# Kernel tuning notes

Measured on AMD Instinct MI355X. Metric: run time of the kernel, lower is better.

Reference implementation:

```python
import jax, jax.numpy as jnp
import numpy as np

T, B, D = 512, 16, 2048


def setup_inputs() -> dict:
    key = jax.random.key(0)
    k1, k2, k3, k4, k5 = jax.random.split(key, 5)
    scale = 1.0 / np.sqrt(D)  # keep tanh pre-activations in a sane range
    return {
        "h0": jax.random.normal(k1, (B, D), dtype=jnp.float32),
        "x": jax.random.normal(k2, (T, B, D), dtype=jnp.float32),
        "Wx": jax.random.normal(k3, (D, D), dtype=jnp.float32) * scale,
        "Wh": jax.random.normal(k4, (D, D), dtype=jnp.float32) * scale,
        "Wo": jax.random.normal(k5, (D, D), dtype=jnp.float32) * scale,
    }


def reference(h0, x, Wx, Wh, Wo):
    # ONNX Scan with 1 state var, 1 scan input (axis 0, forward direction),
    # 1 scan output (stacked on axis 0, forward direction), 3 outer vars.
    # Body: h' = tanh(x_t @ Wx + h @ Wh); y_t = h' @ Wo
    def step(h, x_t):
        h_new = jnp.tanh(x_t @ Wx + h @ Wh)   # [B, D]
        y_t = h_new @ Wo                      # [B, D]
        return h_new, y_t

    h_final, ys = jax.lax.scan(step, h0, x)   # ys: [T, B, D]
    return (h_final, ys)
```

## Files before the change

### kernel.cpp

```cpp
#include <hip/hip_runtime.h>
#include <hip/hip_bf16.h>

#define DD 2048
#define TT 512
#define NBLK 64
#define HF_SLOT 32768
#define KT 64
#define FSTRIDE 16

typedef __attribute__((ext_vector_type(4))) float  f32x4;
typedef __attribute__((ext_vector_type(8))) short  bf16x8;
typedef __attribute__((ext_vector_type(8))) unsigned short u16x8;
typedef unsigned short ushort_t;
typedef unsigned long long u64_t;

__device__ __forceinline__ void gld_lds16(const void* g, void* l) {
    __builtin_amdgcn_global_load_lds(
        (const __attribute__((address_space(1))) unsigned int*)g,
        (__attribute__((address_space(3))) unsigned int*)l, 16, 0, 0);
}

__device__ __forceinline__ ushort_t f2bf(float v) {
    __hip_bfloat16 h = __float2bfloat16(v);
    return *(ushort_t*)&h;
}

__device__ __forceinline__ u64_t llc_load64(const u64_t* p) {
    return __hip_atomic_load(p, __ATOMIC_RELAXED, __HIP_MEMORY_SCOPE_AGENT);
}
__device__ __forceinline__ void llc_store64(u64_t* p, u64_t v) {
    __hip_atomic_store(p, v, __ATOMIC_RELAXED, __HIP_MEMORY_SCOPE_AGENT);
}
__device__ __forceinline__ unsigned llc_load32(const unsigned* p) {
    return __hip_atomic_load(p, __ATOMIC_RELAXED, __HIP_MEMORY_SCOPE_AGENT);
}
__device__ __forceinline__ float llc_loadf(const float* p) {
    return __hip_atomic_load(p, __ATOMIC_RELAXED, __HIP_MEMORY_SCOPE_AGENT);
}

__global__ void conv_frag(const float* __restrict__ src, ushort_t* __restrict__ dst) {
    int id = blockIdx.x * 256 + threadIdx.x;
    int l  = id & 63;
    int sk = (id >> 6) & 63;
    int mt = id >> 12;
    const float* s = src + (size_t)(mt * 16 + (l & 15)) * DD + sk * 32 + ((l >> 4) * 8);
    float4 a = *(const float4*)s;
    float4 b = *(const float4*)(s + 4);
    u16x8 r;
    r[0] = f2bf(a.x); r[1] = f2bf(a.y); r[2] = f2bf(a.z); r[3] = f2bf(a.w);
    r[4] = f2bf(b.x); r[5] = f2bf(b.y); r[6] = f2bf(b.z); r[7] = f2bf(b.w);
    *(u16x8*)(dst + (size_t)id * 8) = r;
}

__global__ void conv_wt(const float* __restrict__ W, ushort_t* __restrict__ Wt) {
    int id = blockIdx.x * 256 + threadIdx.x;
    int n  = id & (DD - 1);
    int k8 = id >> 11;
    u16x8 r;
#pragma unroll
    for (int j = 0; j < 8; ++j)
        r[j] = f2bf(W[(size_t)(k8 * 8 + j) * DD + n]);
    *(u16x8*)(Wt + (size_t)n * DD + k8 * 8) = r;
}

__global__ __launch_bounds__(256) void gemm_frag(
    const ushort_t* __restrict__ Af, const ushort_t* __restrict__ Bt,
    float* __restrict__ C) {
    __shared__ ushort_t lA[8 * 64 * 8];
    __shared__ ushort_t lB[8 * 64 * 8];
    int tid = threadIdx.x;
    int w = tid >> 6, l = tid & 63;
    int wm = w >> 1, wn = w & 1;
    int quad = l >> 4, col = l & 15;
    int mt0 = blockIdx.x * 8;
    int n0  = blockIdx.y * 128;

    f32x4 acc[4][4] = {};

    for (int sk = 0; sk < KT; ++sk) {
        __syncthreads();
#pragma unroll
        for (int q = 0; q < 2; ++q) {
            int i = w * 2 + q;
            const ushort_t* ga = Af + ((size_t)((mt0 + i) * 64 + sk) * 64 + l) * 8;
            gld_lds16(ga, &lA[i * 512]);
            int jt = i;
            const ushort_t* gb = Bt + (size_t)(n0 + jt * 16 + col) * DD + sk * 32 + quad * 8;
            gld_lds16(gb, &lB[jt * 512]);
        }
        __syncthreads();
        bf16x8 af[4], bf[4];
#pragma unroll
        for (int i = 0; i < 4; ++i) af[i] = *(const bf16x8*)&lA[((wm * 4 + i) * 64 + l) * 8];
#pragma unroll
        for (int j = 0; j < 4; ++j) bf[j] = *(const bf16x8*)&lB[((wn * 4 + j) * 64 + l) * 8];
#pragma unroll
        for (int i = 0; i < 4; ++i)
#pragma unroll
            for (int j = 0; j < 4; ++j)
                acc[i][j] = __builtin_amdgcn_mfma_f32_16x16x32_bf16(af[i], bf[j], acc[i][j], 0, 0, 0);
    }

#pragma unroll
    for (int i = 0; i < 4; ++i)
#pragma unroll
        for (int j = 0; j < 4; ++j) {
            int rg0 = (mt0 + wm * 4 + i) * 16 + quad * 4;
            int cg  = n0 + (wn * 4 + j) * 16 + col;
#pragma unroll
            for (int r = 0; r < 4; ++r)
                C[(size_t)(rg0 + r) * DD + cg] = acc[i][j][r];
        }
}

__global__ __launch_bounds__(256, 1) void rnn_fused(
    const ushort_t* __restrict__ Wht,
    const ushort_t* __restrict__ Wot,
    ushort_t* __restrict__ Hf,
    const float* __restrict__ A32,
    float* __restrict__ out,
    unsigned* __restrict__ flags) {
    __shared__ ushort_t lW[4 * 16 * 2 * 512];
    __shared__ float scr[2048];
    __shared__ ushort_t hstage[512];
    int tid = threadIdx.x;
    int w = tid >> 6, l = tid & 63;
    int quad = l >> 4, col = l & 15;
    bool is_rnn = blockIdx.x < NBLK;
    int b = is_rnn ? blockIdx.x : blockIdx.x - NBLK;
    int c0 = b * 32;
    float* ys = out + HF_SLOT;

    const ushort_t* Wsrc = is_rnn ? Wht : Wot;
#pragma unroll
    for (int s = 0; s < 16; ++s) {
        int sk = w * 16 + s;
#pragma unroll
        for (int jt = 0; jt < 2; ++jt) {
            const ushort_t* gb = Wsrc + (size_t)(c0 + jt * 16 + col) * DD + sk * 32 + quad * 8;
            gld_lds16(gb, &lW[((w * 16 + s) * 2 + jt) << 9]);
        }
    }
    __syncthreads();

    for (int t = 1; t <= TT; ++t) {
        float av[4];
        if (is_rnn && w < 2) {
#pragma unroll
            for (int r = 0; r < 4; ++r)
                av[r] = llc_loadf(&A32[(size_t)((t - 1) * 16 + quad * 4 + r) * DD + c0 + w * 16 + col]);
        }

        unsigned tgt = is_rnn ? (unsigned)(t - 1) : (unsigned)t;
        if (w == 3) {
            unsigned f;
            do {
                f = llc_load32(&flags[l * FSTRIDE]);
            } while (!__all((int)(f >= tgt)));
        }
        __syncthreads();

        const ushort_t* hsrc = Hf + (size_t)(is_rnn ? t - 1 : t) * HF_SLOT;
        bf16x8 hv[16];
#pragma unroll
        for (int s = 0; s < 16; ++s) {
            int sk = w * 16 + s;
            const u64_t* p = (const u64_t*)(hsrc + (size_t)(sk * 64 + l) * 8);
            union { u64_t q[2]; bf16x8 v; } u;
            u.q[0] = llc_load64(p);
            u.q[1] = llc_load64(p + 1);
            hv[s] = u.v;
        }

        f32x4 acc0 = {0.f, 0.f, 0.f, 0.f};
        f32x4 acc1 = {0.f, 0.f, 0.f, 0.f};
#pragma unroll
        for (int s = 0; s < 16; ++s) {
            bf16x8 w0 = *(const bf16x8*)&lW[(((w * 16 + s) * 2 + 0) << 9) + l * 8];
            bf16x8 w1 = *(const bf16x8*)&lW[(((w * 16 + s) * 2 + 1) << 9) + l * 8];
            acc0 = __builtin_amdgcn_mfma_f32_16x16x32_bf16(hv[s], w0, acc0, 0, 0, 0);
            acc1 = __builtin_amdgcn_mfma_f32_16x16x32_bf16(hv[s], w1, acc1, 0, 0, 0);
        }
        *(f32x4*)&scr[((w * 2 + 0) * 64 + l) * 4] = acc0;
        *(f32x4*)&scr[((w * 2 + 1) * 64 + l) * 4] = acc1;
        __syncthreads();

        if (w < 2) {
            int jt = w;
            f32x4 p0 = *(f32x4*)&scr[((0 * 2 + jt) * 64 + l) * 4];
            f32x4 p1 = *(f32x4*)&scr[((1 * 2 + jt) * 64 + l) * 4];
            f32x4 p2 = *(f32x4*)&scr[((2 * 2 + jt) * 64 + l) * 4];
            f32x4 p3 = *(f32x4*)&scr[((3 * 2 + jt) * 64 + l) * 4];
            int lc = jt * 16 + col;
            if (is_rnn) {
                int q2 = lc >> 3, jj = lc & 7;
#pragma unroll
                for (int r = 0; r < 4; ++r) {
                    int m = quad * 4 + r;
                    float x = p0[r] + p1[r] + p2[r] + p3[r] + av[r];
                    float e2 = __expf(-2.f * fabsf(x));
                    float th = copysignf((1.f - e2) / (1.f + e2), x);
                    hstage[(q2 * 16 + m) * 8 + jj] = f2bf(th);
                    if (t == TT) out[(size_t)m * DD + c0 + lc] = th;
                }
            } else {
#pragma unroll
                for (int r = 0; r < 4; ++r) {
                    int m = quad * 4 + r;
                    float y = p0[r] + p1[r] + p2[r] + p3[r];
                    ys[(size_t)((t - 1) * 16 + m) * DD + c0 + lc] = y;
                }
            }
        }

        if (is_rnn) {
            __syncthreads();
            if (w == 0) {
                u64_t* dst = (u64_t*)(Hf + (size_t)t * HF_SLOT + (size_t)(c0 >> 5) * 512);
                const u64_t* s = (const u64_t*)hstage;
                llc_store64(dst + l,      s[l]);
                llc_store64(dst + 64 + l, s[64 + l]);
                __builtin_amdgcn_s_waitcnt(0);
                if (l == 0)
                    __hip_atomic_store(&flags[b * FSTRIDE], (unsigned)t,
                                       __ATOMIC_RELAXED, __HIP_MEMORY_SCOPE_AGENT);
            }
        }
    }
}

extern "C" void kernel_launch(void* const* d_in, const int* in_sizes, int n_in,
                              void* d_out, int out_size, void* d_ws, size_t ws_size,
                              hipStream_t stream) {
    const float* h0 = (const float*)d_in[0];
    const float* x  = (const float*)d_in[1];
    const float* Wx = (const float*)d_in[2];
    const float* Wh = (const float*)d_in[3];
    const float* Wo = (const float*)d_in[4];
    float* out = (float*)d_out;

    char* ws = (char*)d_ws;
    unsigned* flags = (unsigned*)ws;
    ushort_t* Hf  = (ushort_t*)(ws + 4096);
    ushort_t* Xf  = Hf + HF_SLOT;
    size_t hf_bytes = (size_t)(TT + 1) * HF_SLOT * 2;
    ushort_t* Wxt = (ushort_t*)(ws + 4096 + hf_bytes);
    ushort_t* Wht = Wxt + (size_t)DD * DD;
    ushort_t* Wot = Wht + (size_t)DD * DD;
    float* A32 = out + HF_SLOT;

    hipMemsetAsync(d_ws, 0, 4096, stream);

    conv_frag<<<8192, 256, 0, stream>>>(x, Xf);
    conv_frag<<<16, 256, 0, stream>>>(h0, Hf);
    conv_wt<<<2048, 256, 0, stream>>>(Wx, Wxt);
    conv_wt<<<2048, 256, 0, stream>>>(Wh, Wht);
    conv_wt<<<2048, 256, 0, stream>>>(Wo, Wot);

    gemm_frag<<<dim3(64, 16), 256, 0, stream>>>(Xf, Wxt, A32);

    rnn_fused<<<2 * NBLK, 256, 0, stream>>>(Wht, Wot, Hf, A32, out, flags);
}
```

Before: 1.914 ms.

## Replace per-block step flags with NaN-sentinel polling on hidden-state data

Drops the flag array and its spin-wait barrier. The hidden-state buffer is pre-filled with a bf16 NaN sentinel, and consumers poll the data itself, running each K-chunk's MFMA as soon as that chunk holds no sentinel. This removes the separate flag store, the waitcnt before it and a block-wide barrier from the per-step critical path, and lets compute overlap with data arriving. The cost is an extra kernel that fills the whole Hf region, including the area aliased with Xf, and repeated polling loads. Correctness depends on tanh outputs never matching the sentinel bit pattern.

```diff
diff --git a/kernel.cpp b/kernel.cpp
--- a/kernel.cpp
+++ b/kernel.cpp
@@ -6,7 +6,7 @@
 #define NBLK 64
 #define HF_SLOT 32768
 #define KT 64
-#define FSTRIDE 16
+#define SENT32 0x7FC07FC0u
 
 typedef __attribute__((ext_vector_type(4))) float  f32x4;
 typedef __attribute__((ext_vector_type(8))) short  bf16x8;
@@ -30,9 +30,6 @@
 }
 __device__ __forceinline__ void llc_store64(u64_t* p, u64_t v) {
     __hip_atomic_store(p, v, __ATOMIC_RELAXED, __HIP_MEMORY_SCOPE_AGENT);
-}
-__device__ __forceinline__ unsigned llc_load32(const unsigned* p) {
-    return __hip_atomic_load(p, __ATOMIC_RELAXED, __HIP_MEMORY_SCOPE_AGENT);
 }
 __device__ __forceinline__ float llc_loadf(const float* p) {
     return __hip_atomic_load(p, __ATOMIC_RELAXED, __HIP_MEMORY_SCOPE_AGENT);
@@ -63,6 +60,13 @@
     *(u16x8*)(Wt + (size_t)n * DD + k8 * 8) = r;
 }
 
+__global__ void fill_sent(u64_t* __restrict__ dst) {
+    size_t id = (size_t)blockIdx.x * 256 + threadIdx.x;
+    u64_t v = 0x7FC07FC07FC07FC0ull;
+    dst[id * 2]     = v;
+    dst[id * 2 + 1] = v;
+}
+
 __global__ __launch_bounds__(256) void gemm_frag(
     const ushort_t* __restrict__ Af, const ushort_t* __restrict__ Bt,
     float* __restrict__ C) {
@@ -118,8 +122,7 @@
     const ushort_t* __restrict__ Wot,
     ushort_t* __restrict__ Hf,
     const float* __restrict__ A32,
-    float* __restrict__ out,
-    unsigned* __restrict__ flags) {
+    float* __restrict__ out) {
     __shared__ ushort_t lW[4 * 16 * 2 * 512];
     __shared__ float scr[2048];
     __shared__ ushort_t hstage[512];
@@ -138,7 +141,7 @@
 #pragma unroll
         for (int jt = 0; jt < 2; ++jt) {
             const ushort_t* gb = Wsrc + (size_t)(c0 + jt * 16 + col) * DD + sk * 32 + quad * 8;
-            gld_lds16(gb, &lW[((w * 16 + s) * 2 + jt) << 9]);
+            gld_lds16(gb, &lW[((sk * 2 + jt) << 9)]);
         }
     }
     __syncthreads();
@@ -151,36 +154,40 @@
                 av[r] = llc_loadf(&A32[(size_t)((t - 1) * 16 + quad * 4 + r) * DD + c0 + w * 16 + col]);
         }
 
-        unsigned tgt = is_rnn ? (unsigned)(t - 1) : (unsigned)t;
-        if (w == 3) {
-            unsigned f;
-            do {
-                f = llc_load32(&flags[l * FSTRIDE]);
-            } while (!__all((int)(f >= tgt)));
-        }
-        __syncthreads();
-
         const ushort_t* hsrc = Hf + (size_t)(is_rnn ? t - 1 : t) * HF_SLOT;
-        bf16x8 hv[16];
-#pragma unroll
-        for (int s = 0; s < 16; ++s) {
-            int sk = w * 16 + s;
-            const u64_t* p = (const u64_t*)(hsrc + (size_t)(sk * 64 + l) * 8);
-            union { u64_t q[2]; bf16x8 v; } u;
-            u.q[0] = llc_load64(p);
-            u.q[1] = llc_load64(p + 1);
-            hv[s] = u.v;
-        }
+        const u64_t* hbase = (const u64_t*)hsrc + ((size_t)(w * 16) * 64 + l) * 2;
 
         f32x4 acc0 = {0.f, 0.f, 0.f, 0.f};
         f32x4 acc1 = {0.f, 0.f, 0.f, 0.f};
-#pragma unroll
-        for (int s = 0; s < 16; ++s) {
-            bf16x8 w0 = *(const bf16x8*)&lW[(((w * 16 + s) * 2 + 0) << 9) + l * 8];
-            bf16x8 w1 = *(const bf16x8*)&lW[(((w * 16 + s) * 2 + 1) << 9) + l * 8];
-            acc0 = __builtin_amdgcn_mfma_f32_16x16x32_bf16(hv[s], w0, acc0, 0, 0, 0);
-            acc1 = __builtin_amdgcn_mfma_f32_16x16x32_bf16(hv[s], w1, acc1, 0, 0, 0);
-        }
+        unsigned pend = 0xFFFFu;
+        while (pend) {
+            u64_t q0[16], q1[16];
+#pragma unroll
+            for (int s = 0; s < 16; ++s)
+                if (pend & (1u << s)) {
+                    const u64_t* p = hbase + (size_t)s * 128;
+                    q0[s] = llc_load64(p);
+                    q1[s] = llc_load64(p + 1);
+                }
+#pragma unroll
+            for (int s = 0; s < 16; ++s)
+                if (pend & (1u << s)) {
+                    unsigned x0 = (unsigned)q0[s], x1 = (unsigned)(q0[s] >> 32);
+                    unsigned x2 = (unsigned)q1[s], x3 = (unsigned)(q1[s] >> 32);
+                    bool ok = (x0 != SENT32) & (x1 != SENT32) & (x2 != SENT32) & (x3 != SENT32);
+                    if (__all((int)ok)) {
+                        pend &= ~(1u << s);
+                        union { u64_t q[2]; bf16x8 v; } u;
+                        u.q[0] = q0[s]; u.q[1] = q1[s];
+                        int sk = w * 16 + s;
+                        bf16x8 w0 = *(const bf16x8*)&lW[((sk * 2 + 0) << 9) + l * 8];
+                        bf16x8 w1 = *(const bf16x8*)&lW[((sk * 2 + 1) << 9) + l * 8];
+                        acc0 = __builtin_amdgcn_mfma_f32_16x16x32_bf16(u.v, w0, acc0, 0, 0, 0);
+                        acc1 = __builtin_amdgcn_mfma_f32_16x16x32_bf16(u.v, w1, acc1, 0, 0, 0);
+                    }
+                }
+        }
+
         *(f32x4*)&scr[((w * 2 + 0) * 64 + l) * 4] = acc0;
         *(f32x4*)&scr[((w * 2 + 1) * 64 + l) * 4] = acc1;
         __syncthreads();
@@ -213,18 +220,13 @@
             }
         }
 
-        if (is_rnn) {
-            __syncthreads();
-            if (w == 0) {
-                u64_t* dst = (u64_t*)(Hf + (size_t)t * HF_SLOT + (size_t)(c0 >> 5) * 512);
-                const u64_t* s = (const u64_t*)hstage;
-                llc_store64(dst + l,      s[l]);
-                llc_store64(dst + 64 + l, s[64 + l]);
-                __builtin_amdgcn_s_waitcnt(0);
-                if (l == 0)
-                    __hip_atomic_store(&flags[b * FSTRIDE], (unsigned)t,
-                                       __ATOMIC_RELAXED, __HIP_MEMORY_SCOPE_AGENT);
-            }
+        __syncthreads();
+
+        if (is_rnn && w == 0) {
+            u64_t* dst = (u64_t*)(Hf + (size_t)t * HF_SLOT + (size_t)(c0 >> 5) * 512);
+            const u64_t* sp = (const u64_t*)hstage;
+            llc_store64(dst + l,      sp[l]);
+            llc_store64(dst + 64 + l, sp[64 + l]);
         }
     }
 }
@@ -240,7 +242,6 @@
     float* out = (float*)d_out;
 
     char* ws = (char*)d_ws;
-    unsigned* flags = (unsigned*)ws;
     ushort_t* Hf  = (ushort_t*)(ws + 4096);
     ushort_t* Xf  = Hf + HF_SLOT;
     size_t hf_bytes = (size_t)(TT + 1) * HF_SLOT * 2;
@@ -249,8 +250,6 @@
     ushort_t* Wot = Wht + (size_t)DD * DD;
     float* A32 = out + HF_SLOT;
 
-    hipMemsetAsync(d_ws, 0, 4096, stream);
-
     conv_frag<<<8192, 256, 0, stream>>>(x, Xf);
     conv_frag<<<16, 256, 0, stream>>>(h0, Hf);
     conv_wt<<<2048, 256, 0, stream>>>(Wx, Wxt);
@@ -259,5 +258,7 @@
 
     gemm_frag<<<dim3(64, 16), 256, 0, stream>>>(Xf, Wxt, A32);
 
-    rnn_fused<<<2 * NBLK, 256, 0, stream>>>(Wht, Wot, Hf, A32, out, flags);
-}
+    fill_sent<<<8192, 256, 0, stream>>>((u64_t*)(Hf + HF_SLOT));
+
+    rnn_fused<<<2 * NBLK, 256, 0, stream>>>(Wht, Wot, Hf, A32, out);
+}
```

Measured after the change: 2.377 ms. 1.24x slower.

## Speculatively prefetch hidden state using NaN sentinels to overlap with flag wait

Applied to the files above, without the earlier changes.

Before the scan kernel runs, every per-step hidden-state slot is filled with a bf16 NaN sentinel pattern. RNN blocks now issue their loads of the previous hidden state before spinning on the cross-block flags. After the barrier they check each fragment for sentinels, consume ready fragments with MFMA, and reload only the missing ones. This is meant to overlap global-load latency with the inter-block synchronisation on the serial critical path. MFMA accumulation is also split into two independent chains to shorten dependency latency. The cost is an extra fill pass of roughly 32 MB, plus polling and branch overhead in the inner loop.

```diff
diff --git a/kernel.cpp b/kernel.cpp
--- a/kernel.cpp
+++ b/kernel.cpp
@@ -7,6 +7,7 @@
 #define HF_SLOT 32768
 #define KT 64
 #define FSTRIDE 16
+#define SENT32 0x7FC07FC0u
 
 typedef __attribute__((ext_vector_type(4))) float  f32x4;
 typedef __attribute__((ext_vector_type(8))) short  bf16x8;
@@ -61,6 +62,13 @@
     for (int j = 0; j < 8; ++j)
         r[j] = f2bf(W[(size_t)(k8 * 8 + j) * DD + n]);
     *(u16x8*)(Wt + (size_t)n * DD + k8 * 8) = r;
+}
+
+__global__ void fill_sent(u64_t* __restrict__ dst) {
+    size_t id = (size_t)blockIdx.x * 256 + threadIdx.x;
+    u64_t v = 0x7FC07FC07FC07FC0ull;
+    dst[id * 2]     = v;
+    dst[id * 2 + 1] = v;
 }
 
 __global__ __launch_bounds__(256) void gemm_frag(
@@ -144,55 +152,80 @@
     __syncthreads();
 
     for (int t = 1; t <= TT; ++t) {
-        float av[4];
-        if (is_rnn && w < 2) {
-#pragma unroll
-            for (int r = 0; r < 4; ++r)
-                av[r] = llc_loadf(&A32[(size_t)((t - 1) * 16 + quad * 4 + r) * DD + c0 + w * 16 + col]);
-        }
-
-        unsigned tgt = is_rnn ? (unsigned)(t - 1) : (unsigned)t;
-        if (w == 3) {
-            unsigned f;
-            do {
-                f = llc_load32(&flags[l * FSTRIDE]);
-            } while (!__all((int)(f >= tgt)));
-        }
-        __syncthreads();
-
-        const ushort_t* hsrc = Hf + (size_t)(is_rnn ? t - 1 : t) * HF_SLOT;
-        bf16x8 hv[16];
-#pragma unroll
-        for (int s = 0; s < 16; ++s) {
-            int sk = w * 16 + s;
-            const u64_t* p = (const u64_t*)(hsrc + (size_t)(sk * 64 + l) * 8);
-            union { u64_t q[2]; bf16x8 v; } u;
-            u.q[0] = llc_load64(p);
-            u.q[1] = llc_load64(p + 1);
-            hv[s] = u.v;
-        }
-
         f32x4 acc0 = {0.f, 0.f, 0.f, 0.f};
         f32x4 acc1 = {0.f, 0.f, 0.f, 0.f};
-#pragma unroll
-        for (int s = 0; s < 16; ++s) {
-            bf16x8 w0 = *(const bf16x8*)&lW[(((w * 16 + s) * 2 + 0) << 9) + l * 8];
-            bf16x8 w1 = *(const bf16x8*)&lW[(((w * 16 + s) * 2 + 1) << 9) + l * 8];
-            acc0 = __builtin_amdgcn_mfma_f32_16x16x32_bf16(hv[s], w0, acc0, 0, 0, 0);
-            acc1 = __builtin_amdgcn_mfma_f32_16x16x32_bf16(hv[s], w1, acc1, 0, 0, 0);
-        }
-        *(f32x4*)&scr[((w * 2 + 0) * 64 + l) * 4] = acc0;
-        *(f32x4*)&scr[((w * 2 + 1) * 64 + l) * 4] = acc1;
-        __syncthreads();
-
-        if (w < 2) {
-            int jt = w;
-            f32x4 p0 = *(f32x4*)&scr[((0 * 2 + jt) * 64 + l) * 4];
-            f32x4 p1 = *(f32x4*)&scr[((1 * 2 + jt) * 64 + l) * 4];
-            f32x4 p2 = *(f32x4*)&scr[((2 * 2 + jt) * 64 + l) * 4];
-            f32x4 p3 = *(f32x4*)&scr[((3 * 2 + jt) * 64 + l) * 4];
-            int lc = jt * 16 + col;
-            if (is_rnn) {
+
+        if (is_rnn) {
+            float av[4];
+            if (w < 2) {
+#pragma unroll
+                for (int r = 0; r < 4; ++r)
+                    av[r] = llc_loadf(&A32[(size_t)((t - 1) * 16 + quad * 4 + r) * DD + c0 + w * 16 + col]);
+            }
+            const ushort_t* hsrc = Hf + (size_t)(t - 1) * HF_SLOT;
+            const u64_t* hq = (const u64_t*)hsrc + ((size_t)(w * 16) * 64 + l) * 2;
+            u64_t q0[16], q1[16];
+#pragma unroll
+            for (int s = 0; s < 16; ++s) {
+                q0[s] = llc_load64(hq + (size_t)s * 128);
+                q1[s] = llc_load64(hq + (size_t)s * 128 + 1);
+            }
+
+            if (w == 3) {
+                unsigned f;
+                do {
+                    f = llc_load32(&flags[l * FSTRIDE]);
+                } while (!__all((int)(f >= (unsigned)(t - 1))));
+            }
+            __syncthreads();
+
+            f32x4 aB0 = {0.f, 0.f, 0.f, 0.f};
+            f32x4 aB1 = {0.f, 0.f, 0.f, 0.f};
+            unsigned pend = 0xFFFFu;
+            while (pend) {
+#pragma unroll
+                for (int s = 0; s < 16; ++s)
+                    if (pend & (1u << s)) {
+                        unsigned x0 = (unsigned)q0[s], x1 = (unsigned)(q0[s] >> 32);
+                        unsigned x2 = (unsigned)q1[s], x3 = (unsigned)(q1[s] >> 32);
+                        bool ok = (x0 != SENT32) & (x1 != SENT32) & (x2 != SENT32) & (x3 != SENT32);
+                        if (__all((int)ok)) {
+                            pend &= ~(1u << s);
+                            union { u64_t q[2]; bf16x8 v; } u;
+                            u.q[0] = q0[s]; u.q[1] = q1[s];
+                            int sk = w * 16 + s;
+                            bf16x8 w0 = *(const bf16x8*)&lW[((sk * 2 + 0) << 9) + l * 8];
+                            bf16x8 w1 = *(const bf16x8*)&lW[((sk * 2 + 1) << 9) + l * 8];
+                            if (s & 1) {
+                                aB0 = __builtin_amdgcn_mfma_f32_16x16x32_bf16(u.v, w0, aB0, 0, 0, 0);
+                                aB1 = __builtin_amdgcn_mfma_f32_16x16x32_bf16(u.v, w1, aB1, 0, 0, 0);
+                            } else {
+                                acc0 = __builtin_amdgcn_mfma_f32_16x16x32_bf16(u.v, w0, acc0, 0, 0, 0);
+                                acc1 = __builtin_amdgcn_mfma_f32_16x16x32_bf16(u.v, w1, acc1, 0, 0, 0);
+                            }
+                        }
+                    }
+#pragma unroll
+                for (int s = 0; s < 16; ++s)
+                    if (pend & (1u << s)) {
+                        q0[s] = llc_load64(hq + (size_t)s * 128);
+                        q1[s] = llc_load64(hq + (size_t)s * 128 + 1);
+                    }
+            }
+            acc0 = acc0 + aB0;
+            acc1 = acc1 + aB1;
+
+            *(f32x4*)&scr[((w * 2 + 0) * 64 + l) * 4] = acc0;
+            *(f32x4*)&scr[((w * 2 + 1) * 64 + l) * 4] = acc1;
+            __syncthreads();
+
+            if (w < 2) {
+                int jt = w;
+                f32x4 p0 = *(f32x4*)&scr[((0 * 2 + jt) * 64 + l) * 4];
+                f32x4 p1 = *(f32x4*)&scr[((1 * 2 + jt) * 64 + l) * 4];
+                f32x4 p2 = *(f32x4*)&scr[((2 * 2 + jt) * 64 + l) * 4];
+                f32x4 p3 = *(f32x4*)&scr[((3 * 2 + jt) * 64 + l) * 4];
+                int lc = jt * 16 + col;
                 int q2 = lc >> 3, jj = lc & 7;
 #pragma unroll
                 for (int r = 0; r < 4; ++r) {
@@ -203,27 +236,72 @@
                     hstage[(q2 * 16 + m) * 8 + jj] = f2bf(th);
                     if (t == TT) out[(size_t)m * DD + c0 + lc] = th;
                 }
-            } else {
+            }
+            __syncthreads();
+            if (w == 0) {
+                u64_t* dst = (u64_t*)(Hf + (size_t)t * HF_SLOT + (size_t)b * 512);
+                const u64_t* sp = (const u64_t*)hstage;
+                llc_store64(dst + l,      sp[l]);
+                llc_store64(dst + 64 + l, sp[64 + l]);
+                __builtin_amdgcn_s_waitcnt(0);
+                if (l == 0)
+                    __hip_atomic_store(&flags[b * FSTRIDE], (unsigned)t,
+                                       __ATOMIC_RELAXED, __HIP_MEMORY_SCOPE_AGENT);
+            }
+        } else {
+            if (w == 3) {
+                unsigned f;
+                do {
+                    f = llc_load32(&flags[l * FSTRIDE]);
+                } while (!__all((int)(f >= (unsigned)t)));
+            }
+            __syncthreads();
+
+            const ushort_t* hsrc = Hf + (size_t)t * HF_SLOT;
+            bf16x8 hv[16];
+#pragma unroll
+            for (int s = 0; s < 16; ++s) {
+                int sk = w * 16 + s;
+                const u64_t* p = (const u64_t*)(hsrc + (size_t)(sk * 64 + l) * 8);
+                union { u64_t q[2]; bf16x8 v; } u;
+                u.q[0] = llc_load64(p);
+                u.q[1] = llc_load64(p + 1);
+                hv[s] = u.v;
+            }
+            f32x4 aB0 = {0.f, 0.f, 0.f, 0.f};
+            f32x4 aB1 = {0.f, 0.f, 0.f, 0.f};
+#pragma unroll
+            for (int s = 0; s < 16; ++s) {
+                bf16x8 w0 = *(const bf16x8*)&lW[(((w * 16 + s) * 2 + 0) << 9) + l * 8];
+                bf16x8 w1 = *(const bf16x8*)&lW[(((w * 16 + s) * 2 + 1) << 9) + l * 8];
+                if (s & 1) {
+                    aB0 = __builtin_amdgcn_mfma_f32_16x16x32_bf16(hv[s], w0, aB0, 0, 0, 0);
+                    aB1 = __builtin_amdgcn_mfma_f32_16x16x32_bf16(hv[s], w1, aB1, 0, 0, 0);
+                } else {
+                    acc0 = __builtin_amdgcn_mfma_f32_16x16x32_bf16(hv[s], w0, acc0, 0, 0, 0);
+                    acc1 = __builtin_amdgcn_mfma_f32_16x16x32_bf16(hv[s], w1, acc1, 0, 0, 0);
+                }
+            }
+            acc0 = acc0 + aB0;
+            acc1 = acc1 + aB1;
+
+            *(f32x4*)&scr[((w * 2 + 0) * 64 + l) * 4] = acc0;
+            *(f32x4*)&scr[((w * 2 + 1) * 64 + l) * 4] = acc1;
+            __syncthreads();
+
+            if (w < 2) {
+                int jt = w;
+                f32x4 p0 = *(f32x4*)&scr[((0 * 2 + jt) * 64 + l) * 4];
+                f32x4 p1 = *(f32x4*)&scr[((1 * 2 + jt) * 64 + l) * 4];
+                f32x4 p2 = *(f32x4*)&scr[((2 * 2 + jt) * 64 + l) * 4];
+                f32x4 p3 = *(f32x4*)&scr[((3 * 2 + jt) * 64 + l) * 4];
+                int lc = jt * 16 + col;
 #pragma unroll
                 for (int r = 0; r < 4; ++r) {
                     int m = quad * 4 + r;
                     float y = p0[r] + p1[r] + p2[r] + p3[r];
                     ys[(size_t)((t - 1) * 16 + m) * DD + c0 + lc] = y;
                 }
-            }
-        }
-
-        if (is_rnn) {
-            __syncthreads();
-            if (w == 0) {
-                u64_t* dst = (u64_t*)(Hf + (size_t)t * HF_SLOT + (size_t)(c0 >> 5) * 512);
-                const u64_t* s = (const u64_t*)hstage;
-                llc_store64(dst + l,      s[l]);
-                llc_store64(dst + 64 + l, s[64 + l]);
-                __builtin_amdgcn_s_waitcnt(0);
-                if (l == 0)
-                    __hip_atomic_store(&flags[b * FSTRIDE], (unsigned)t,
-                                       __ATOMIC_RELAXED, __HIP_MEMORY_SCOPE_AGENT);
             }
         }
     }
@@ -259,5 +337,7 @@
 
     gemm_frag<<<dim3(64, 16), 256, 0, stream>>>(Xf, Wxt, A32);
 
+    fill_sent<<<8192, 256, 0, stream>>>((u64_t*)(Hf + HF_SLOT));
+
     rnn_fused<<<2 * NBLK, 256, 0, stream>>>(Wht, Wot, Hf, A32, out, flags);
 }
```

Result: slower. 3.027 ms (+58.2%).

## Split output projection out of recurrent kernel into a separate batched GEMM

Applied to the files above, without the earlier changes.

Removes the 64 output-projection blocks that ran alongside the recurrence step by step. After the recurrent kernel finishes, all hidden states are multiplied by Wo in one large GEMM. The recurrent kernel keeps only the serial h@Wh work, which frees CUs and L2 bandwidth on the critical path and makes the output projection a dense parallel GEMM. The cost is that the projection no longer overlaps with the recurrence, and A32 and ys share the same buffer, which stays correct only because of kernel ordering.

```diff
diff --git a/kernel.cpp b/kernel.cpp
--- a/kernel.cpp
+++ b/kernel.cpp
@@ -113,9 +113,8 @@
         }
 }
 
-__global__ __launch_bounds__(256, 1) void rnn_fused(
+__global__ __launch_bounds__(256, 1) void rnn_ring(
     const ushort_t* __restrict__ Wht,
-    const ushort_t* __restrict__ Wot,
     ushort_t* __restrict__ Hf,
     const float* __restrict__ A32,
     float* __restrict__ out,
@@ -126,18 +125,15 @@
     int tid = threadIdx.x;
     int w = tid >> 6, l = tid & 63;
     int quad = l >> 4, col = l & 15;
-    bool is_rnn = blockIdx.x < NBLK;
-    int b = is_rnn ? blockIdx.x : blockIdx.x - NBLK;
+    int b = blockIdx.x;
     int c0 = b * 32;
-    float* ys = out + HF_SLOT;
-
-    const ushort_t* Wsrc = is_rnn ? Wht : Wot;
+
 #pragma unroll
     for (int s = 0; s < 16; ++s) {
         int sk = w * 16 + s;
 #pragma unroll
         for (int jt = 0; jt < 2; ++jt) {
-            const ushort_t* gb = Wsrc + (size_t)(c0 + jt * 16 + col) * DD + sk * 32 + quad * 8;
+            const ushort_t* gb = Wht + (size_t)(c0 + jt * 16 + col) * DD + sk * 32 + quad * 8;
             gld_lds16(gb, &lW[((w * 16 + s) * 2 + jt) << 9]);
         }
     }
@@ -145,22 +141,21 @@
 
     for (int t = 1; t <= TT; ++t) {
         float av[4];
-        if (is_rnn && w < 2) {
+        if (w < 2) {
 #pragma unroll
             for (int r = 0; r < 4; ++r)
                 av[r] = llc_loadf(&A32[(size_t)((t - 1) * 16 + quad * 4 + r) * DD + c0 + w * 16 + col]);
         }
 
-        unsigned tgt = is_rnn ? (unsigned)(t - 1) : (unsigned)t;
         if (w == 3) {
             unsigned f;
             do {
                 f = llc_load32(&flags[l * FSTRIDE]);
-            } while (!__all((int)(f >= tgt)));
-        }
-        __syncthreads();
-
-        const ushort_t* hsrc = Hf + (size_t)(is_rnn ? t - 1 : t) * HF_SLOT;
+            } while (!__all((int)(f >= (unsigned)(t - 1))));
+        }
+        __syncthreads();
+
+        const ushort_t* hsrc = Hf + (size_t)(t - 1) * HF_SLOT;
         bf16x8 hv[16];
 #pragma unroll
         for (int s = 0; s < 16; ++s) {
@@ -192,39 +187,27 @@
             f32x4 p2 = *(f32x4*)&scr[((2 * 2 + jt) * 64 + l) * 4];
             f32x4 p3 = *(f32x4*)&scr[((3 * 2 + jt) * 64 + l) * 4];
             int lc = jt * 16 + col;
-            if (is_rnn) {
-                int q2 = lc >> 3, jj = lc & 7;
-#pragma unroll
-                for (int r = 0; r < 4; ++r) {
-                    int m = quad * 4 + r;
-                    float x = p0[r] + p1[r] + p2[r] + p3[r] + av[r];
-                    float e2 = __expf(-2.f * fabsf(x));
-                    float th = copysignf((1.f - e2) / (1.f + e2), x);
-                    hstage[(q2 * 16 + m) * 8 + jj] = f2bf(th);
-                    if (t == TT) out[(size_t)m * DD + c0 + lc] = th;
-                }
-            } else {
-#pragma unroll
-                for (int r = 0; r < 4; ++r) {
-                    int m = quad * 4 + r;
-                    float y = p0[r] + p1[r] + p2[r] + p3[r];
-                    ys[(size_t)((t - 1) * 16 + m) * DD + c0 + lc] = y;
-                }
+            int q2 = lc >> 3, jj = lc & 7;
+#pragma unroll
+            for (int r = 0; r < 4; ++r) {
+                int m = quad * 4 + r;
+                float x = p0[r] + p1[r] + p2[r] + p3[r] + av[r];
+                float e2 = __expf(-2.f * fabsf(x));
+                float th = copysignf((1.f - e2) / (1.f + e2), x);
+                hstage[(q2 * 16 + m) * 8 + jj] = f2bf(th);
+                if (t == TT) out[(size_t)m * DD + c0 + lc] = th;
             }
         }
-
-        if (is_rnn) {
-            __syncthreads();
-            if (w == 0) {
-                u64_t* dst = (u64_t*)(Hf + (size_t)t * HF_SLOT + (size_t)(c0 >> 5) * 512);
-                const u64_t* s = (const u64_t*)hstage;
-                llc_store64(dst + l,      s[l]);
-                llc_store64(dst + 64 + l, s[64 + l]);
-                __builtin_amdgcn_s_waitcnt(0);
-                if (l == 0)
-                    __hip_atomic_store(&flags[b * FSTRIDE], (unsigned)t,
-                                       __ATOMIC_RELAXED, __HIP_MEMORY_SCOPE_AGENT);
-            }
+        __syncthreads();
+        if (w == 0) {
+            u64_t* dst = (u64_t*)(Hf + (size_t)t * HF_SLOT + (size_t)b * 512);
+            const u64_t* sp = (const u64_t*)hstage;
+            llc_store64(dst + l,      sp[l]);
+            llc_store64(dst + 64 + l, sp[64 + l]);
+            __builtin_amdgcn_s_waitcnt(0);
+            if (l == 0)
+                __hip_atomic_store(&flags[b * FSTRIDE], (unsigned)t,
+                                   __ATOMIC_RELAXED, __HIP_MEMORY_SCOPE_AGENT);
         }
     }
 }
@@ -248,6 +231,7 @@
     ushort_t* Wht = Wxt + (size_t)DD * DD;
     ushort_t* Wot = Wht + (size_t)DD * DD;
     float* A32 = out + HF_SLOT;
+    float* ys  = out + HF_SLOT;
 
     hipMemsetAsync(d_ws, 0, 4096, stream);
 
@@ -259,5 +243,7 @@
 
     gemm_frag<<<dim3(64, 16), 256, 0, stream>>>(Xf, Wxt, A32);
 
-    rnn_fused<<<2 * NBLK, 256, 0, stream>>>(Wht, Wot, Hf, A32, out, flags);
-}
+    rnn_ring<<<NBLK, 256, 0, stream>>>(Wht, Hf, A32, out, flags);
+
+    gemm_frag<<<dim3(64, 16), 256, 0, stream>>>(Hf + HF_SLOT, Wot, ys);
+}
```

New measurement: 2.058 ms. +7.6%, slower.
